# Optimization experiments

Measured on AMD Instinct MI355X. Metric: run time of the kernel, lower is better.

Reference implementation:

```python
import jax, jax.numpy as jnp
import numpy as np

K, N, GROUP = 4096, 12288, 64
M = 4096  # tokens (batch*seq)


def setup_inputs() -> dict:
    key = jax.random.key(0)
    k1, k2, k3, k4, k5 = jax.random.split(key, 5)
    input = jax.random.normal(k1, (M, K), dtype=jnp.float32)
    qweight = jax.random.randint(k2, (K, N), 0, 4, dtype=jnp.int32)  # int2 codes in [0,4)
    scale = jax.random.uniform(k3, (K // GROUP, N), dtype=jnp.float32)
    zp = jax.random.normal(k4, (K // GROUP, N), dtype=jnp.float32)
    bias = jax.random.normal(k5, (N,), dtype=jnp.float32)
    return {"input": input, "qweight": qweight, "scale": scale, "zp": zp, "bias": bias}


def reference(input, qweight, scale, zp, bias):
    # Group-wise asymmetric dequant: W[k,n] = q[k,n]*scale[k//g,n] + zp[k//g,n]
    G = K // GROUP
    q = qweight.astype(input.dtype).reshape(G, GROUP, N)
    w = q * scale[:, None, :] + zp[:, None, :]          # [G, g, N]
    w = w.reshape(K, N)
    out = input @ w + bias[None, :]                      # [M, N]
    return out
```

## Files before the change

### kernel.cpp

```cpp
#include <hip/hip_runtime.h>
#include <hip/hip_bf16.h>

#define Mdim 4096
#define Kdim 4096
#define Ndim 12288

typedef __attribute__((ext_vector_type(8))) short short8;
typedef __attribute__((ext_vector_type(4))) float floatx4;
typedef __attribute__((ext_vector_type(4))) int intx4;
typedef __attribute__((ext_vector_type(4))) unsigned short ushortx4;
typedef __attribute__((ext_vector_type(8))) unsigned short ushortx8;

static __device__ __forceinline__ unsigned short f2bf(float x) {
    __hip_bfloat16 h = __float2bfloat16(x);
    return __builtin_bit_cast(unsigned short, h);
}

static __device__ __forceinline__ void gload_lds16(const unsigned short* g, unsigned short* l) {
    __builtin_amdgcn_global_load_lds(
        (const __attribute__((address_space(1))) unsigned int*)g,
        (__attribute__((address_space(3))) unsigned int*)l,
        16, 0, 0);
}

__global__ void __launch_bounds__(256)
dequant_transpose(const int* __restrict__ Q, const float* __restrict__ S,
                  const float* __restrict__ Z, unsigned short* __restrict__ Wt)
{
    __shared__ unsigned short Ls[64][72];
    const int t     = threadIdx.x;
    const int kbase = blockIdx.x * 256;
    const int n0    = blockIdx.y * 64;
    const int tn = t & 15, tk = t >> 4;
    const int nc = tn * 4;
    const int n_out  = t >> 2;
    const int kc_out = (t & 3) * 16;

    #pragma unroll
    for (int s = 0; s < 4; ++s) {
        const int k0 = kbase + s * 64;
        const int g  = k0 >> 6;
        const floatx4 s4 = *reinterpret_cast<const floatx4*>(&S[(size_t)g * Ndim + n0 + nc]);
        const floatx4 z4 = *reinterpret_cast<const floatx4*>(&Z[(size_t)g * Ndim + n0 + nc]);
        intx4 q[4];
        #pragma unroll
        for (int r = 0; r < 4; ++r)
            q[r] = *reinterpret_cast<const intx4*>(&Q[(size_t)(k0 + tk * 4 + r) * Ndim + n0 + nc]);
        if (s) __syncthreads();
        #pragma unroll
        for (int j = 0; j < 4; ++j) {
            const float sv = s4[j], zv = z4[j];
            ushortx4 w;
            w.x = f2bf(fmaf((float)q[0][j], sv, zv));
            w.y = f2bf(fmaf((float)q[1][j], sv, zv));
            w.z = f2bf(fmaf((float)q[2][j], sv, zv));
            w.w = f2bf(fmaf((float)q[3][j], sv, zv));
            *reinterpret_cast<ushortx4*>(&Ls[nc + j][tk * 4]) = w;
        }
        __syncthreads();
        const ushortx8 a = *reinterpret_cast<const ushortx8*>(&Ls[n_out][kc_out]);
        const ushortx8 b = *reinterpret_cast<const ushortx8*>(&Ls[n_out][kc_out + 8]);
        unsigned short* dst = &Wt[(size_t)(n0 + n_out) * Kdim + k0 + kc_out];
        *reinterpret_cast<ushortx8*>(dst)     = a;
        *reinterpret_cast<ushortx8*>(dst + 8) = b;
    }
}

__global__ void __launch_bounds__(256)
xconv(const float* __restrict__ X, unsigned short* __restrict__ Xw)
{
    const size_t i = ((size_t)blockIdx.x * 256 + threadIdx.x) * 8;
    const floatx4 a = *reinterpret_cast<const floatx4*>(&X[i]);
    const floatx4 b = *reinterpret_cast<const floatx4*>(&X[i + 4]);
    ushortx8 w;
    w[0] = f2bf(a.x); w[1] = f2bf(a.y); w[2] = f2bf(a.z); w[3] = f2bf(a.w);
    w[4] = f2bf(b.x); w[5] = f2bf(b.y); w[6] = f2bf(b.z); w[7] = f2bf(b.w);
    *reinterpret_cast<ushortx8*>(&Xw[i]) = w;
}


#define STAGE_A(c, kt, h) do { \
    const unsigned short* sp_ = A + aoff + (size_t)((h) * 128) * Kdim + (size_t)(kt) * 64; \
    unsigned short* dp_ = &As[c][((h) * 128 + wave * 16) * 64]; \
    gload_lds16(sp_, dp_); \
    gload_lds16(sp_ + (size_t)8 * Kdim, dp_ + 8 * 64); \
} while (0)

#define STAGE_B(c, kt, h) do { \
    const unsigned short* sp_ = B + boff + (size_t)((h) * 128) * Kdim + (size_t)(kt) * 64; \
    unsigned short* dp_ = &Bs[c][((h) * 128 + wave * 16) * 64]; \
    gload_lds16(sp_, dp_); \
    gload_lds16(sp_ + (size_t)8 * Kdim, dp_ + 8 * 64); \
} while (0)

#define LDA_(c, i, kh) (*reinterpret_cast<const short8*>( \
    &As[c][(wm + (i) * 16 + lrow) * 64 + (((kh) * 4 + quad) ^ lsw) * 8]))
#define LDB_(c, j, kh) (*reinterpret_cast<const short8*>( \
    &Bs[c][(wn + (j) * 16 + lrow) * 64 + (((kh) * 4 + quad) ^ lsw) * 8]))

#define PHASE_SYNC() do { \
    __builtin_amdgcn_s_barrier(); \
    asm volatile("s_waitcnt lgkmcnt(0)" ::: "memory"); \
    __builtin_amdgcn_sched_barrier(0); \
} while (0)

#define MFMA_QUAD(ILO, JO) do { \
    __builtin_amdgcn_s_setprio(1); \
    _Pragma("unroll") \
    for (int i_ = 0; i_ < 4; ++i_) { \
        _Pragma("unroll") \
        for (int jj_ = 0; jj_ < 2; ++jj_) { \
            acc[(ILO) + i_][(JO) + jj_] = __builtin_amdgcn_mfma_f32_16x16x32_bf16( \
                af[(ILO) + i_][0], bfr[jj_][0], acc[(ILO) + i_][(JO) + jj_], 0, 0, 0); \
            acc[(ILO) + i_][(JO) + jj_] = __builtin_amdgcn_mfma_f32_16x16x32_bf16( \
                af[(ILO) + i_][1], bfr[jj_][1], acc[(ILO) + i_][(JO) + jj_], 0, 0, 0); \
        } \
    } \
    __builtin_amdgcn_s_setprio(0); \
} while (0)

__global__ void __launch_bounds__(512, 2)
gemm_bf16_8p(const unsigned short* __restrict__ A, const unsigned short* __restrict__ B,
             const float* __restrict__ bias, float* __restrict__ O)
{
    __shared__ unsigned short As[2][256 * 64];
    __shared__ unsigned short Bs[2][256 * 64];

    constexpr int NT = Kdim / 64;

    const int nblk = Ndim / 256;
    const int cpx  = (Mdim / 256) * nblk / 8;
    const int bid  = blockIdx.x;
    const int swz  = (bid & 7) * cpx + (bid >> 3);
    const int gsz  = 8 * nblk;
    const int grp  = swz / gsz;
    const int r    = swz % gsz;
    const int m0   = (grp * 8 + (r & 7)) * 256;
    const int n0   = (r >> 3) * 256;

    const int t    = threadIdx.x;
    const int wave = t >> 6;
    const int lane = t & 63;
    const int wm   = (wave >> 2) * 128;
    const int wn   = (wave & 3) * 64;
    const int lrow = lane & 15;
    const int quad = lane >> 4;
    const int lsw  = lrow & 7;

    const int srow = lane >> 3;
    const int scol = ((lane & 7) ^ srow) * 8;
    const size_t aoff = (size_t)(m0 + wave * 16 + srow) * Kdim + scol;
    const size_t boff = (size_t)(n0 + wave * 16 + srow) * Kdim + scol;

    floatx4 acc[8][4];
    #pragma unroll
    for (int i = 0; i < 8; ++i)
        #pragma unroll
        for (int j = 0; j < 4; ++j)
            acc[i][j] = floatx4{0.f, 0.f, 0.f, 0.f};

    short8 af[8][2];
    short8 bfr[2][2];

    STAGE_A(0, 0, 0); STAGE_A(0, 0, 1);
    STAGE_B(0, 0, 0); STAGE_B(0, 0, 1);
    STAGE_A(1, 1, 0); STAGE_A(1, 1, 1);
    asm volatile("s_waitcnt vmcnt(4)" ::: "memory");
    __builtin_amdgcn_s_barrier();
    __builtin_amdgcn_sched_barrier(0);

    for (int u = 0; u < NT; ++u) {
        const int c = u & 1;

        #pragma unroll
        for (int i = 0; i < 4; ++i) { af[i][0] = LDA_(c, i, 0); af[i][1] = LDA_(c, i, 1); }
        #pragma unroll
        for (int j = 0; j < 2; ++j) { bfr[j][0] = LDB_(c, j, 0); bfr[j][1] = LDB_(c, j, 1); }
        if (u + 1 < NT) STAGE_B(c ^ 1, u + 1, 0);
        PHASE_SYNC();
        MFMA_QUAD(0, 0);
        __builtin_amdgcn_s_barrier();

        #pragma unroll
        for (int i = 4; i < 8; ++i) { af[i][0] = LDA_(c, i, 0); af[i][1] = LDA_(c, i, 1); }
        if (u + 1 < NT) STAGE_B(c ^ 1, u + 1, 1);
        PHASE_SYNC();
        MFMA_QUAD(4, 0);
        __builtin_amdgcn_s_barrier();

        #pragma unroll
        for (int j = 0; j < 2; ++j) { bfr[j][0] = LDB_(c, j + 2, 0); bfr[j][1] = LDB_(c, j + 2, 1); }
        if (u + 2 < NT) STAGE_A(c, u + 2, 0);
        PHASE_SYNC();
        MFMA_QUAD(0, 2);
        __builtin_amdgcn_s_barrier();

        if (u + 2 < NT) STAGE_A(c, u + 2, 1);
        MFMA_QUAD(4, 2);
        if (u < NT - 2) { asm volatile("s_waitcnt vmcnt(4)" ::: "memory"); }
        else            { asm volatile("s_waitcnt vmcnt(0)" ::: "memory"); }
        __builtin_amdgcn_s_barrier();
        __builtin_amdgcn_sched_barrier(0);
    }

    #pragma unroll
    for (int j = 0; j < 4; ++j) {
        const int col = n0 + wn + j * 16 + lrow;
        const float bv = bias[col];
        #pragma unroll
        for (int i = 0; i < 8; ++i) {
            const int rbase = m0 + wm + i * 16 + quad * 4;
            #pragma unroll
            for (int rr = 0; rr < 4; ++rr)
                O[(size_t)(rbase + rr) * Ndim + col] = acc[i][j][rr] + bv;
        }
    }
}

__global__ void __launch_bounds__(256)
w2a16_gemm_fb(const float* __restrict__ X, const int* __restrict__ Q,
              const float* __restrict__ S, const float* __restrict__ Z,
              const float* __restrict__ bias, float* __restrict__ O)
{
    __shared__ unsigned short Asf[128][72];
    __shared__ unsigned short Bsf[128][72];
    const int t  = threadIdx.x;
    const int n0 = blockIdx.x * 128;
    const int m0 = blockIdx.y * 128;
    const int wave = t >> 6, lane = t & 63;
    const int wm = (wave & 1) * 64, wn = (wave >> 1) * 64;
    const int lrow = lane & 15, quad = lane >> 4;
    floatx4 acc[4][4];
    #pragma unroll
    for (int i = 0; i < 4; ++i)
        #pragma unroll
        for (int j = 0; j < 4; ++j) acc[i][j] = floatx4{0.f, 0.f, 0.f, 0.f};
    const int a_row0 = t >> 4, a_c = (t & 15) * 4;
    const int b_n = t & 127, b_k0 = (t >> 7) * 32;
    for (int k0 = 0; k0 < Kdim; k0 += 64) {
        #pragma unroll
        for (int i = 0; i < 8; ++i) {
            const int row = a_row0 + i * 16;
            const floatx4 v = *reinterpret_cast<const floatx4*>(
                &X[(size_t)(m0 + row) * Kdim + k0 + a_c]);
            ushortx4 w;
            w.x = f2bf(v.x); w.y = f2bf(v.y); w.z = f2bf(v.z); w.w = f2bf(v.w);
            *reinterpret_cast<ushortx4*>(&Asf[row][a_c]) = w;
        }
        const int g = k0 >> 6;
        const float s = S[(size_t)g * Ndim + n0 + b_n];
        const float z = Z[(size_t)g * Ndim + n0 + b_n];
        #pragma unroll
        for (int i = 0; i < 8; ++i) {
            const int kk = b_k0 + i * 4;
            const int* qp = &Q[(size_t)(k0 + kk) * Ndim + n0 + b_n];
            ushortx4 w;
            w.x = f2bf(fmaf((float)qp[0],                s, z));
            w.y = f2bf(fmaf((float)qp[(size_t)Ndim],     s, z));
            w.z = f2bf(fmaf((float)qp[(size_t)2 * Ndim], s, z));
            w.w = f2bf(fmaf((float)qp[(size_t)3 * Ndim], s, z));
            *reinterpret_cast<ushortx4*>(&Bsf[b_n][kk]) = w;
        }
        __syncthreads();
        #pragma unroll
        for (int kk = 0; kk < 64; kk += 32) {
            short8 afv[4], bfv[4];
            #pragma unroll
            for (int i = 0; i < 4; ++i)
                afv[i] = *reinterpret_cast<const short8*>(&Asf[wm + i * 16 + lrow][kk + quad * 8]);
            #pragma unroll
            for (int j = 0; j < 4; ++j)
                bfv[j] = *reinterpret_cast<const short8*>(&Bsf[wn + j * 16 + lrow][kk + quad * 8]);
            #pragma unroll
            for (int i = 0; i < 4; ++i)
                #pragma unroll
                for (int j = 0; j < 4; ++j)
                    acc[i][j] = __builtin_amdgcn_mfma_f32_16x16x32_bf16(afv[i], bfv[j], acc[i][j], 0, 0, 0);
        }
        __syncthreads();
    }
    #pragma unroll
    for (int j = 0; j < 4; ++j) {
        const int col = n0 + wn + j * 16 + lrow;
        const float bv = bias[col];
        #pragma unroll
        for (int i = 0; i < 4; ++i) {
            const int rbase = m0 + wm + i * 16 + quad * 4;
            #pragma unroll
            for (int rr = 0; rr < 4; ++rr)
                O[(size_t)(rbase + rr) * Ndim + col] = acc[i][j][rr] + bv;
        }
    }
}

extern "C" void kernel_launch(void* const* d_in, const int* in_sizes, int n_in,
                              void* d_out, int out_size, void* d_ws, size_t ws_size,
                              hipStream_t stream) {
    const float* X  = (const float*)d_in[0];
    const int*   Q  = (const int*)d_in[1];
    const float* S  = (const float*)d_in[2];
    const float* Z  = (const float*)d_in[3];
    const float* Bi = (const float*)d_in[4];
    float* O = (float*)d_out;

    const size_t wt_bytes = (size_t)Kdim * Ndim * 2;
    const size_t xw_bytes = (size_t)Mdim * Kdim * 2;

    if (ws_size >= wt_bytes + xw_bytes) {
        unsigned short* Wt = (unsigned short*)d_ws;
        unsigned short* Xw = (unsigned short*)((char*)d_ws + wt_bytes);

        dim3 g1(Kdim / 256, Ndim / 64);
        hipLaunchKernelGGL(dequant_transpose, g1, dim3(256), 0, stream, Q, S, Z, Wt);

        const int xblocks = (Mdim * Kdim) / (256 * 8);
        hipLaunchKernelGGL(xconv, dim3(xblocks), dim3(256), 0, stream, X, Xw);

        const int nblocks = (Mdim / 256) * (Ndim / 256);
        hipLaunchKernelGGL(gemm_bf16_8p, dim3(nblocks), dim3(512), 0, stream, Xw, Wt, Bi, O);
    } else {
        dim3 grid(Ndim / 128, Mdim / 128);
        hipLaunchKernelGGL(w2a16_gemm_fb, grid, dim3(256), 0, stream, X, Q, S, Z, Bi, O);
    }
}
```

Baseline: 790.6 us.

## Double-buffer register fragments and overlap LDS reads with MFMA in GEMM loop

Restructures the main loop of the bf16 GEMM kernel so A and B register fragments are split into two sets (afA/afB, bA/bB). LDS reads for the next phase or next k-tile now run while MFMAs on the current fragments execute, replacing the old pattern of waiting on lgkmcnt before each MFMA quad. The global-to-LDS staging order is also reshuffled: B is prefetched two tiles ahead and A one tile ahead. This is meant to hide LDS latency behind matrix math, at the cost of more registers and a more delicate barrier/waitcnt schedule where a mistake could cause races.

After: 768.8 us. 1.03x faster.

```diff
diff --git a/kernel.cpp b/kernel.cpp
--- a/kernel.cpp
+++ b/kernel.cpp
@@ -98,22 +98,19 @@
 #define LDB_(c, j, kh) (*reinterpret_cast<const short8*>( \
     &Bs[c][(wn + (j) * 16 + lrow) * 64 + (((kh) * 4 + quad) ^ lsw) * 8]))
 
-#define PHASE_SYNC() do { \
-    __builtin_amdgcn_s_barrier(); \
-    asm volatile("s_waitcnt lgkmcnt(0)" ::: "memory"); \
-    __builtin_amdgcn_sched_barrier(0); \
-} while (0)
-
-#define MFMA_QUAD(ILO, JO) do { \
+#define SBAR()  __builtin_amdgcn_sched_barrier(0)
+
+#define MFMA_Q(AF, BF, IO, JO) do { \
     __builtin_amdgcn_s_setprio(1); \
     _Pragma("unroll") \
-    for (int i_ = 0; i_ < 4; ++i_) { \
+    for (int kh_ = 0; kh_ < 2; ++kh_) { \
         _Pragma("unroll") \
-        for (int jj_ = 0; jj_ < 2; ++jj_) { \
-            acc[(ILO) + i_][(JO) + jj_] = __builtin_amdgcn_mfma_f32_16x16x32_bf16( \
-                af[(ILO) + i_][0], bfr[jj_][0], acc[(ILO) + i_][(JO) + jj_], 0, 0, 0); \
-            acc[(ILO) + i_][(JO) + jj_] = __builtin_amdgcn_mfma_f32_16x16x32_bf16( \
-                af[(ILO) + i_][1], bfr[jj_][1], acc[(ILO) + i_][(JO) + jj_], 0, 0, 0); \
+        for (int i_ = 0; i_ < 4; ++i_) { \
+            _Pragma("unroll") \
+            for (int j_ = 0; j_ < 2; ++j_) { \
+                acc[(IO) + i_][(JO) + j_] = __builtin_amdgcn_mfma_f32_16x16x32_bf16( \
+                    AF[i_][kh_], BF[j_][kh_], acc[(IO) + i_][(JO) + j_], 0, 0, 0); \
+            } \
         } \
     } \
     __builtin_amdgcn_s_setprio(0); \
@@ -159,48 +156,73 @@
         for (int j = 0; j < 4; ++j)
             acc[i][j] = floatx4{0.f, 0.f, 0.f, 0.f};
 
-    short8 af[8][2];
-    short8 bfr[2][2];
+    short8 afA[4][2];
+    short8 afB[4][2];
+    short8 bA[2][2];
+    short8 bB[2][2];
 
     STAGE_A(0, 0, 0); STAGE_A(0, 0, 1);
     STAGE_B(0, 0, 0); STAGE_B(0, 0, 1);
-    STAGE_A(1, 1, 0); STAGE_A(1, 1, 1);
-    asm volatile("s_waitcnt vmcnt(4)" ::: "memory");
+    STAGE_B(1, 1, 0); STAGE_B(1, 1, 1);
+    STAGE_A(1, 1, 0);
+    asm volatile("s_waitcnt vmcnt(2)" ::: "memory");
     __builtin_amdgcn_s_barrier();
-    __builtin_amdgcn_sched_barrier(0);
+    SBAR();
+    #pragma unroll
+    for (int i = 0; i < 4; ++i) { afA[i][0] = LDA_(0, i, 0); afA[i][1] = LDA_(0, i, 1); }
+    #pragma unroll
+    for (int j = 0; j < 2; ++j) { bA[j][0] = LDB_(0, j, 0); bA[j][1] = LDB_(0, j, 1); }
+    #pragma unroll
+    for (int j = 0; j < 2; ++j) { bB[j][0] = LDB_(0, j + 2, 0); bB[j][1] = LDB_(0, j + 2, 1); }
+    asm volatile("s_waitcnt lgkmcnt(0)" ::: "memory");
+    SBAR();
+    __builtin_amdgcn_s_barrier();
+    SBAR();
 
     for (int u = 0; u < NT; ++u) {
-        const int c = u & 1;
-
-        #pragma unroll
-        for (int i = 0; i < 4; ++i) { af[i][0] = LDA_(c, i, 0); af[i][1] = LDA_(c, i, 1); }
-        #pragma unroll
-        for (int j = 0; j < 2; ++j) { bfr[j][0] = LDB_(c, j, 0); bfr[j][1] = LDB_(c, j, 1); }
-        if (u + 1 < NT) STAGE_B(c ^ 1, u + 1, 0);
-        PHASE_SYNC();
-        MFMA_QUAD(0, 0);
+        const int c = u & 1, cn = c ^ 1;
+
+        #pragma unroll
+        for (int i = 0; i < 4; ++i) { afB[i][0] = LDA_(c, i + 4, 0); afB[i][1] = LDA_(c, i + 4, 1); }
+        if (u + 1 < NT) STAGE_A(cn, u + 1, 1);
+        if (u + 2 < NT) STAGE_B(c, u + 2, 0);
+        MFMA_Q(afA, bA, 0, 0);
+        SBAR();
         __builtin_amdgcn_s_barrier();
-
-        #pragma unroll
-        for (int i = 4; i < 8; ++i) { af[i][0] = LDA_(c, i, 0); af[i][1] = LDA_(c, i, 1); }
-        if (u + 1 < NT) STAGE_B(c ^ 1, u + 1, 1);
-        PHASE_SYNC();
-        MFMA_QUAD(4, 0);
-        __builtin_amdgcn_s_barrier();
-
-        #pragma unroll
-        for (int j = 0; j < 2; ++j) { bfr[j][0] = LDB_(c, j + 2, 0); bfr[j][1] = LDB_(c, j + 2, 1); }
-        if (u + 2 < NT) STAGE_A(c, u + 2, 0);
-        PHASE_SYNC();
-        MFMA_QUAD(0, 2);
-        __builtin_amdgcn_s_barrier();
-
-        if (u + 2 < NT) STAGE_A(c, u + 2, 1);
-        MFMA_QUAD(4, 2);
+        SBAR();
+
+        if (u + 2 < NT) STAGE_B(c, u + 2, 1);
+        MFMA_Q(afB, bA, 4, 0);
+        SBAR();
         if (u < NT - 2) { asm volatile("s_waitcnt vmcnt(4)" ::: "memory"); }
         else            { asm volatile("s_waitcnt vmcnt(0)" ::: "memory"); }
         __builtin_amdgcn_s_barrier();
-        __builtin_amdgcn_sched_barrier(0);
+        SBAR();
+
+        if (u + 1 < NT) {
+            #pragma unroll
+            for (int j = 0; j < 2; ++j) { bA[j][0] = LDB_(cn, j, 0); bA[j][1] = LDB_(cn, j, 1); }
+        }
+        MFMA_Q(afA, bB, 0, 2);
+        SBAR();
+        __builtin_amdgcn_s_barrier();
+        SBAR();
+
+        if (u + 1 < NT) {
+            #pragma unroll
+            for (int i = 0; i < 4; ++i) { afA[i][0] = LDA_(cn, i, 0); afA[i][1] = LDA_(cn, i, 1); }
+        }
+        if (u + 2 < NT) STAGE_A(c, u + 2, 0);
+        MFMA_Q(afB, bB, 4, 2);
+        SBAR();
+        if (u + 1 < NT) {
+            #pragma unroll
+            for (int j = 0; j < 2; ++j) { bB[j][0] = LDB_(cn, j + 2, 0); bB[j][1] = LDB_(cn, j + 2, 1); }
+        }
+        asm volatile("s_waitcnt lgkmcnt(0)" ::: "memory");
+        SBAR();
+        __builtin_amdgcn_s_barrier();
+        SBAR();
     }
 
     #pragma unroll
```
